# Kernel optimization log

Measured on AMD Instinct MI355X. Metric: run time of the kernel, lower is better.

## Reference

```python
import jax, jax.numpy as jnp
import numpy as np

B, J, D = 64, 512, 1024

def setup_inputs() -> dict:
    key = jax.random.key(0)
    k_x, k_m, k1, k2, k3 = jax.random.split(key, 5)
    x = jax.random.normal(k_x, (B, J, D), dtype=jnp.float32)
    mask = (jax.random.uniform(k_m, (B, J)) > 0.1).astype(jnp.float32)
    s1 = 1.0 / np.sqrt(D)
    W1 = jax.random.uniform(k1, (D, D), minval=-s1, maxval=s1, dtype=jnp.float32)
    b1 = jnp.zeros((D,), jnp.float32)
    W2 = jax.random.uniform(k2, (D, 1), minval=-s1, maxval=s1, dtype=jnp.float32)
    b2 = jnp.zeros((1,), jnp.float32)
    W3 = jax.random.uniform(k3, (D, 3), minval=-s1, maxval=s1, dtype=jnp.float32)
    b3 = jnp.zeros((3,), jnp.float32)
    return {"x": x, "mask": mask, "W1": W1, "b1": b1, "W2": W2, "b2": b2, "W3": W3, "b3": b3}

def reference(x, mask, W1, b1, W2, b2, W3, b3):
    # MLP attention scoring: linear1 -> tanh -> linear2 -> sigmoid
    h = jnp.tanh(jnp.einsum('bjd,de->bje', x, W1) + b1)          # [B,J,D]
    val = jax.nn.sigmoid(jnp.einsum('bjd,do->bjo', h, W2) + b2)  # [B,J,1]
    val = val * mask[:, :, None]                                  # mask out pads
    inv_sum = 1.0 / jnp.sum(val, axis=(1, 2))                     # [B]
    att_weights = val * inv_sum[:, None, None]                    # [B,J,1]
    pooled = jnp.einsum('bjk,bjm->bk', x, att_weights)            # [B,D]
    output_val = pooled @ W3 + b3                                 # [B,3]
    return output_val, att_weights
```

## Files before the change

kernel.cpp:

```cpp
#include <hip/hip_runtime.h>
#include <math.h>
#include <stdint.h>

#define B_ 64
#define J_ 512
#define D_ 1024

typedef __attribute__((ext_vector_type(8))) short short8;
typedef __attribute__((ext_vector_type(4))) float f32x4;

#define GLOBAL_AS __attribute__((address_space(1)))
#define LDS_AS    __attribute__((address_space(3)))

__device__ __forceinline__ void async16(const void* g, void* l) {
    __builtin_amdgcn_global_load_lds((const GLOBAL_AS uint32_t*)g,
                                     (LDS_AS uint32_t*)l, 16, 0, 0);
}

__device__ __forceinline__ float fast_tanh(float x) {
    return 1.0f - 2.0f / (1.0f + __expf(2.0f * x));
}

__device__ __forceinline__ uint32_t f2bf(float f) {
    uint32_t u = __builtin_bit_cast(uint32_t, f);
    u += 0x7fffu + ((u >> 16) & 1u);
    return u >> 16;
}
__device__ __forceinline__ uint32_t pack2(float lo, float hi) {
    return f2bf(lo) | (f2bf(hi) << 16);
}

__global__ __launch_bounds__(256) void transpose_cast_w1(const float* __restrict__ W1,
                                                         unsigned short* __restrict__ W1t) {
    __shared__ float t[32][33];
    const int n = blockIdx.x * 32 + threadIdx.x;
    for (int i = threadIdx.y; i < 32; i += 8)
        t[i][threadIdx.x] = W1[(size_t)(blockIdx.y * 32 + i) * D_ + n];
    __syncthreads();
    const int k = blockIdx.y * 32 + threadIdx.x;
    for (int i = threadIdx.y; i < 32; i += 8)
        W1t[(size_t)(blockIdx.x * 32 + i) * D_ + k] =
            (unsigned short)f2bf(t[threadIdx.x][i]);
}

__global__ __launch_bounds__(256, 2) void gemm_score_kernel(
    const float* __restrict__ x, const unsigned short* __restrict__ W1t,
    const float* __restrict__ b1, const float* __restrict__ W2,
    const float* __restrict__ b2, const float* __restrict__ mask,
    float* __restrict__ val_ws, float* __restrict__ pooled_part)
{
    __shared__ __align__(16) unsigned short ldsA[64 * 64];
    __shared__ __align__(16) unsigned short ldsB[256 * 64];
    __shared__ float pv_part[4][64];
    __shared__ float vrow[64];

    const int tid  = threadIdx.x;
    const int wave = tid >> 6;
    const int l    = tid & 63;
    const int l15  = l & 15;
    const int kgrp = l >> 4;
    const int l7   = l & 7;
    const int r0   = blockIdx.x * 64;

    const int ar = tid >> 3;
    const int ac = tid & 7;
    const float* gA0 = x + (size_t)(r0 + ar) * D_ + (ac << 3);
    const float* gA1 = gA0 + (size_t)32 * D_;
    uint4* dA0 = (uint4*)(ldsA + ar * 64 + ((ac ^ (ar & 7)) << 3));
    uint4* dA1 = (uint4*)(ldsA + (ar + 32) * 64 + ((ac ^ (ar & 7)) << 3));

    const int brl  = l >> 3;
    const int blog = (l & 7) ^ brl;
    size_t gBoff[8];
    unsigned short* lB[8];
    #pragma unroll
    for (int t = 0; t < 8; ++t) {
        const int row = t * 32 + wave * 8 + brl;
        gBoff[t] = (size_t)row * D_ + (blog << 3);
        lB[t] = ldsB + t * 2048 + wave * 512;
    }

    int aoff[4][2], boff[4][2];
    #pragma unroll
    for (int mi = 0; mi < 4; ++mi)
        #pragma unroll
        for (int ks = 0; ks < 2; ++ks)
            aoff[mi][ks] = (mi * 16 + l15) * 64 + (((ks * 4 + kgrp) ^ l7) << 3);
    #pragma unroll
    for (int ni = 0; ni < 4; ++ni)
        #pragma unroll
        for (int ks = 0; ks < 2; ++ks) {
            const int row = wave * 64 + ni * 16 + l15;
            boff[ni][ks] = row * 64 + (((ks * 4 + kgrp) ^ l7) << 3);
        }

    float pv[4][4];
    #pragma unroll
    for (int mi = 0; mi < 4; ++mi)
        #pragma unroll
        for (int r = 0; r < 4; ++r) pv[mi][r] = 0.f;

    for (int n0 = 0; n0 < 4; ++n0) {
        f32x4 acc[4][4];
        #pragma unroll
        for (int mi = 0; mi < 4; ++mi)
            #pragma unroll
            for (int ni = 0; ni < 4; ++ni)
                acc[mi][ni] = (f32x4){0.f, 0.f, 0.f, 0.f};

        const size_t nofs = (size_t)n0 * 256 * D_;
        for (int k0 = 0; k0 < D_; k0 += 64) {
            const float4 a00 = *reinterpret_cast<const float4*>(gA0 + k0);
            const float4 a01 = *reinterpret_cast<const float4*>(gA0 + k0 + 4);
            const float4 a10 = *reinterpret_cast<const float4*>(gA1 + k0);
            const float4 a11 = *reinterpret_cast<const float4*>(gA1 + k0 + 4);
            uint4 p0, p1;
            p0.x = pack2(a00.x, a00.y); p0.y = pack2(a00.z, a00.w);
            p0.z = pack2(a01.x, a01.y); p0.w = pack2(a01.z, a01.w);
            p1.x = pack2(a10.x, a10.y); p1.y = pack2(a10.z, a10.w);
            p1.z = pack2(a11.x, a11.y); p1.w = pack2(a11.z, a11.w);
            *dA0 = p0;
            *dA1 = p1;
            #pragma unroll
            for (int t = 0; t < 8; ++t)
                async16(W1t + nofs + gBoff[t] + k0, lB[t]);
            __syncthreads();

            #pragma unroll
            for (int ks = 0; ks < 2; ++ks) {
                short8 af[4], bfr[4];
                #pragma unroll
                for (int mi = 0; mi < 4; ++mi)
                    af[mi] = *reinterpret_cast<const short8*>(ldsA + aoff[mi][ks]);
                #pragma unroll
                for (int ni = 0; ni < 4; ++ni)
                    bfr[ni] = *reinterpret_cast<const short8*>(ldsB + boff[ni][ks]);
                #pragma unroll
                for (int mi = 0; mi < 4; ++mi)
                    #pragma unroll
                    for (int ni = 0; ni < 4; ++ni)
                        acc[mi][ni] = __builtin_amdgcn_mfma_f32_16x16x32_bf16(
                            af[mi], bfr[ni], acc[mi][ni], 0, 0, 0);
            }
            __syncthreads();
        }

        #pragma unroll
        for (int ni = 0; ni < 4; ++ni) {
            const int col = n0 * 256 + wave * 64 + ni * 16 + l15;
            const float b1v = b1[col];
            const float w2v = W2[col];
            #pragma unroll
            for (int mi = 0; mi < 4; ++mi)
                #pragma unroll
                for (int r = 0; r < 4; ++r) {
                    const float h = fast_tanh(acc[mi][ni][r] + b1v);
                    pv[mi][r] = fmaf(h, w2v, pv[mi][r]);
                }
        }
    }

    #pragma unroll
    for (int mi = 0; mi < 4; ++mi)
        #pragma unroll
        for (int r = 0; r < 4; ++r) {
            float s = pv[mi][r];
            s += __shfl_xor(s, 1);
            s += __shfl_xor(s, 2);
            s += __shfl_xor(s, 4);
            s += __shfl_xor(s, 8);
            if (l15 == 0) pv_part[wave][mi * 16 + kgrp * 4 + r] = s;
        }
    __syncthreads();
    if (tid < 64) {
        float s = b2[0];
        #pragma unroll
        for (int w = 0; w < 4; ++w) s += pv_part[w][tid];
        const float sg = 1.0f / (1.0f + __expf(-s));
        const float v = sg * mask[r0 + tid];
        val_ws[r0 + tid] = v;
        vrow[tid] = v;
    }
    __syncthreads();

    {
        const int kc = tid << 2;
        float a0 = 0.f, a1 = 0.f, a2 = 0.f, a3 = 0.f;
        for (int row = 0; row < 64; ++row) {
            const float v = vrow[row];
            const float4 xv = *reinterpret_cast<const float4*>(
                x + (size_t)(r0 + row) * D_ + kc);
            a0 = fmaf(xv.x, v, a0);
            a1 = fmaf(xv.y, v, a1);
            a2 = fmaf(xv.z, v, a2);
            a3 = fmaf(xv.w, v, a3);
        }
        *reinterpret_cast<float4*>(pooled_part + (size_t)blockIdx.x * D_ + kc) =
            make_float4(a0, a1, a2, a3);
    }
}

__global__ __launch_bounds__(256) void finalize_kernel(
    const float* __restrict__ val_ws, const float* __restrict__ pooled_part,
    const float* __restrict__ W3, const float* __restrict__ b3,
    float* __restrict__ out)
{
    __shared__ float sred[256];
    const int b = blockIdx.x;
    const int tid = threadIdx.x;

    const float v0 = val_ws[b * J_ + tid];
    const float v1 = val_ws[b * J_ + 256 + tid];
    sred[tid] = v0 + v1;
    __syncthreads();
    for (int s = 128; s > 0; s >>= 1) {
        if (tid < s) sred[tid] += sred[tid + s];
        __syncthreads();
    }
    const float inv = 1.0f / sred[0];

    out[192 + b * J_ + tid]       = v0 * inv;
    out[192 + b * J_ + 256 + tid] = v1 * inv;

    const int k = tid << 2;
    float acc3[3] = {0.f, 0.f, 0.f};
    #pragma unroll
    for (int c = 0; c < 4; ++c) {
        float p = 0.f;
        #pragma unroll
        for (int i = 0; i < 8; ++i)
            p += pooled_part[(size_t)(b * 8 + i) * D_ + k + c];
        p *= inv;
        acc3[0] = fmaf(p, W3[(k + c) * 3 + 0], acc3[0]);
        acc3[1] = fmaf(p, W3[(k + c) * 3 + 1], acc3[1]);
        acc3[2] = fmaf(p, W3[(k + c) * 3 + 2], acc3[2]);
    }
    for (int o = 0; o < 3; ++o) {
        __syncthreads();
        sred[tid] = acc3[o];
        __syncthreads();
        for (int s = 128; s > 0; s >>= 1) {
            if (tid < s) sred[tid] += sred[tid + s];
            __syncthreads();
        }
        if (tid == 0) out[b * 3 + o] = sred[0] + b3[o];
    }
}

extern "C" void kernel_launch(void* const* d_in, const int* in_sizes, int n_in,
                              void* d_out, int out_size, void* d_ws, size_t ws_size,
                              hipStream_t stream) {
    const float* x    = (const float*)d_in[0];
    const float* mask = (const float*)d_in[1];
    const float* W1   = (const float*)d_in[2];
    const float* b1   = (const float*)d_in[3];
    const float* W2   = (const float*)d_in[4];
    const float* b2   = (const float*)d_in[5];
    const float* W3   = (const float*)d_in[6];
    const float* b3   = (const float*)d_in[7];
    float* out = (float*)d_out;

    unsigned short* W1t = (unsigned short*)d_ws;
    float* val_ws       = (float*)((char*)d_ws + 2097152);
    float* pooled_part  = (float*)((char*)d_ws + 2097152 + 131072);

    transpose_cast_w1<<<dim3(32, 32), dim3(32, 8), 0, stream>>>(W1, W1t);
    gemm_score_kernel<<<512, 256, 0, stream>>>(x, W1t, b1, W2, b2, mask,
                                               val_ws, pooled_part);
    finalize_kernel<<<B_, 256, 0, stream>>>(val_ws, pooled_part, W3, b3, out);
}
```

Baseline: 321.1 us.

## Fuse finalize into GEMM via last-block counter, prefetch A, vectorize transpose

The separate finalize kernel is removed. The last of the 8 GEMM blocks per batch, found with an atomic counter that the transpose kernel zeroes, now does the normalization and the W3 projection. The A-tile global loads are software-prefetched one k-step ahead, so their latency overlaps the MFMA work. The W1 transpose/cast kernel now uses 64x64 tiles with float4 loads and 16-byte bf16 stores, and the per-tile B address arrays are collapsed into a single base pointer to free registers. The changes save one kernel launch at the cost of threadfences and an atomic, and the prefetch adds register pressure.

New measurement: 401.3 us. 1.25x slower.

```diff
diff --git a/kernel.cpp b/kernel.cpp
--- a/kernel.cpp
+++ b/kernel.cpp
@@ -30,29 +30,58 @@
     return f2bf(lo) | (f2bf(hi) << 16);
 }
 
-__global__ __launch_bounds__(256) void transpose_cast_w1(const float* __restrict__ W1,
-                                                         unsigned short* __restrict__ W1t) {
-    __shared__ float t[32][33];
-    const int n = blockIdx.x * 32 + threadIdx.x;
-    for (int i = threadIdx.y; i < 32; i += 8)
-        t[i][threadIdx.x] = W1[(size_t)(blockIdx.y * 32 + i) * D_ + n];
-    __syncthreads();
-    const int k = blockIdx.y * 32 + threadIdx.x;
-    for (int i = threadIdx.y; i < 32; i += 8)
-        W1t[(size_t)(blockIdx.x * 32 + i) * D_ + k] =
-            (unsigned short)f2bf(t[threadIdx.x][i]);
+__global__ __launch_bounds__(256) void transpose_cast_w1(
+    const float* __restrict__ W1, unsigned short* __restrict__ W1t,
+    unsigned int* __restrict__ cnt)
+{
+    if (blockIdx.x == 0 && blockIdx.y == 0 && threadIdx.x < B_)
+        cnt[threadIdx.x] = 0u;
+
+    __shared__ float t[64][65];
+    const int tx = threadIdx.x;
+    const int k0 = blockIdx.y * 64;
+    const int n0 = blockIdx.x * 64;
+
+    const int kr = tx >> 4;
+    const int c4 = (tx & 15) << 2;
+    #pragma unroll
+    for (int j = 0; j < 4; ++j) {
+        const float4 v = *reinterpret_cast<const float4*>(
+            &W1[(size_t)(k0 + kr + 16 * j) * D_ + n0 + c4]);
+        t[kr + 16 * j][c4 + 0] = v.x;
+        t[kr + 16 * j][c4 + 1] = v.y;
+        t[kr + 16 * j][c4 + 2] = v.z;
+        t[kr + 16 * j][c4 + 3] = v.w;
+    }
+    __syncthreads();
+
+    const int nl = tx >> 3;
+    const int k8 = (tx & 7) << 3;
+    #pragma unroll
+    for (int s = 0; s < 2; ++s) {
+        const int n = nl + 32 * s;
+        uint4 o;
+        o.x = pack2(t[k8 + 0][n], t[k8 + 1][n]);
+        o.y = pack2(t[k8 + 2][n], t[k8 + 3][n]);
+        o.z = pack2(t[k8 + 4][n], t[k8 + 5][n]);
+        o.w = pack2(t[k8 + 6][n], t[k8 + 7][n]);
+        *reinterpret_cast<uint4*>(&W1t[(size_t)(n0 + n) * D_ + k0 + k8]) = o;
+    }
 }
 
 __global__ __launch_bounds__(256, 2) void gemm_score_kernel(
     const float* __restrict__ x, const unsigned short* __restrict__ W1t,
     const float* __restrict__ b1, const float* __restrict__ W2,
     const float* __restrict__ b2, const float* __restrict__ mask,
-    float* __restrict__ val_ws, float* __restrict__ pooled_part)
+    const float* __restrict__ W3, const float* __restrict__ b3,
+    float* __restrict__ out, float* __restrict__ val_ws,
+    float* __restrict__ pooled_part, unsigned int* __restrict__ cnt)
 {
     __shared__ __align__(16) unsigned short ldsA[64 * 64];
     __shared__ __align__(16) unsigned short ldsB[256 * 64];
     __shared__ float pv_part[4][64];
     __shared__ float vrow[64];
+    __shared__ int lastflag;
 
     const int tid  = threadIdx.x;
     const int wave = tid >> 6;
@@ -61,6 +90,7 @@
     const int kgrp = l >> 4;
     const int l7   = l & 7;
     const int r0   = blockIdx.x * 64;
+    const int bb   = r0 >> 9;
 
     const int ar = tid >> 3;
     const int ac = tid & 7;
@@ -71,14 +101,8 @@
 
     const int brl  = l >> 3;
     const int blog = (l & 7) ^ brl;
-    size_t gBoff[8];
-    unsigned short* lB[8];
-    #pragma unroll
-    for (int t = 0; t < 8; ++t) {
-        const int row = t * 32 + wave * 8 + brl;
-        gBoff[t] = (size_t)row * D_ + (blog << 3);
-        lB[t] = ldsB + t * 2048 + wave * 512;
-    }
+    const unsigned short* gBbase = W1t + (size_t)(wave * 8 + brl) * D_ + (blog << 3);
+    unsigned short* lBbase = ldsB + wave * 512;
 
     int aoff[4][2], boff[4][2];
     #pragma unroll
@@ -100,6 +124,11 @@
         #pragma unroll
         for (int r = 0; r < 4; ++r) pv[mi][r] = 0.f;
 
+    float4 pa00 = *reinterpret_cast<const float4*>(gA0);
+    float4 pa01 = *reinterpret_cast<const float4*>(gA0 + 4);
+    float4 pa10 = *reinterpret_cast<const float4*>(gA1);
+    float4 pa11 = *reinterpret_cast<const float4*>(gA1 + 4);
+
     for (int n0 = 0; n0 < 4; ++n0) {
         f32x4 acc[4][4];
         #pragma unroll
@@ -110,21 +139,24 @@
 
         const size_t nofs = (size_t)n0 * 256 * D_;
         for (int k0 = 0; k0 < D_; k0 += 64) {
-            const float4 a00 = *reinterpret_cast<const float4*>(gA0 + k0);
-            const float4 a01 = *reinterpret_cast<const float4*>(gA0 + k0 + 4);
-            const float4 a10 = *reinterpret_cast<const float4*>(gA1 + k0);
-            const float4 a11 = *reinterpret_cast<const float4*>(gA1 + k0 + 4);
             uint4 p0, p1;
-            p0.x = pack2(a00.x, a00.y); p0.y = pack2(a00.z, a00.w);
-            p0.z = pack2(a01.x, a01.y); p0.w = pack2(a01.z, a01.w);
-            p1.x = pack2(a10.x, a10.y); p1.y = pack2(a10.z, a10.w);
-            p1.z = pack2(a11.x, a11.y); p1.w = pack2(a11.z, a11.w);
+            p0.x = pack2(pa00.x, pa00.y); p0.y = pack2(pa00.z, pa00.w);
+            p0.z = pack2(pa01.x, pa01.y); p0.w = pack2(pa01.z, pa01.w);
+            p1.x = pack2(pa10.x, pa10.y); p1.y = pack2(pa10.z, pa10.w);
+            p1.z = pack2(pa11.x, pa11.y); p1.w = pack2(pa11.z, pa11.w);
             *dA0 = p0;
             *dA1 = p1;
             #pragma unroll
             for (int t = 0; t < 8; ++t)
-                async16(W1t + nofs + gBoff[t] + k0, lB[t]);
-            __syncthreads();
+                async16(gBbase + nofs + (size_t)t * 32 * D_ + k0,
+                        lBbase + t * 2048);
+            __syncthreads();
+
+            const int nk = (k0 + 64) & (D_ - 1);
+            pa00 = *reinterpret_cast<const float4*>(gA0 + nk);
+            pa01 = *reinterpret_cast<const float4*>(gA0 + nk + 4);
+            pa10 = *reinterpret_cast<const float4*>(gA1 + nk);
+            pa11 = *reinterpret_cast<const float4*>(gA1 + nk + 4);
 
             #pragma unroll
             for (int ks = 0; ks < 2; ++ks) {
@@ -198,52 +230,57 @@
         *reinterpret_cast<float4*>(pooled_part + (size_t)blockIdx.x * D_ + kc) =
             make_float4(a0, a1, a2, a3);
     }
-}
-
-__global__ __launch_bounds__(256) void finalize_kernel(
-    const float* __restrict__ val_ws, const float* __restrict__ pooled_part,
-    const float* __restrict__ W3, const float* __restrict__ b3,
-    float* __restrict__ out)
-{
-    __shared__ float sred[256];
-    const int b = blockIdx.x;
-    const int tid = threadIdx.x;
-
-    const float v0 = val_ws[b * J_ + tid];
-    const float v1 = val_ws[b * J_ + 256 + tid];
-    sred[tid] = v0 + v1;
-    __syncthreads();
-    for (int s = 128; s > 0; s >>= 1) {
-        if (tid < s) sred[tid] += sred[tid + s];
-        __syncthreads();
-    }
-    const float inv = 1.0f / sred[0];
-
-    out[192 + b * J_ + tid]       = v0 * inv;
-    out[192 + b * J_ + 256 + tid] = v1 * inv;
-
-    const int k = tid << 2;
-    float acc3[3] = {0.f, 0.f, 0.f};
-    #pragma unroll
-    for (int c = 0; c < 4; ++c) {
-        float p = 0.f;
-        #pragma unroll
-        for (int i = 0; i < 8; ++i)
-            p += pooled_part[(size_t)(b * 8 + i) * D_ + k + c];
-        p *= inv;
-        acc3[0] = fmaf(p, W3[(k + c) * 3 + 0], acc3[0]);
-        acc3[1] = fmaf(p, W3[(k + c) * 3 + 1], acc3[1]);
-        acc3[2] = fmaf(p, W3[(k + c) * 3 + 2], acc3[2]);
-    }
-    for (int o = 0; o < 3; ++o) {
-        __syncthreads();
-        sred[tid] = acc3[o];
+
+    __threadfence();
+    __syncthreads();
+    if (tid == 0) {
+        const unsigned int old = atomicAdd(&cnt[bb], 1u);
+        lastflag = (old == 7u) ? 1 : 0;
+    }
+    __syncthreads();
+    if (!lastflag) return;
+    __threadfence();
+
+    {
+        float* sred = &pv_part[0][0];
+        const int b = bb;
+
+        const float v0 = val_ws[b * J_ + tid];
+        const float v1 = val_ws[b * J_ + 256 + tid];
+        sred[tid] = v0 + v1;
         __syncthreads();
         for (int s = 128; s > 0; s >>= 1) {
             if (tid < s) sred[tid] += sred[tid + s];
             __syncthreads();
         }
-        if (tid == 0) out[b * 3 + o] = sred[0] + b3[o];
+        const float inv = 1.0f / sred[0];
+
+        out[192 + b * J_ + tid]       = v0 * inv;
+        out[192 + b * J_ + 256 + tid] = v1 * inv;
+
+        const int k = tid << 2;
+        float acc3[3] = {0.f, 0.f, 0.f};
+        #pragma unroll
+        for (int c = 0; c < 4; ++c) {
+            float p = 0.f;
+            #pragma unroll
+            for (int i = 0; i < 8; ++i)
+                p += pooled_part[(size_t)(b * 8 + i) * D_ + k + c];
+            p *= inv;
+            acc3[0] = fmaf(p, W3[(k + c) * 3 + 0], acc3[0]);
+            acc3[1] = fmaf(p, W3[(k + c) * 3 + 1], acc3[1]);
+            acc3[2] = fmaf(p, W3[(k + c) * 3 + 2], acc3[2]);
+        }
+        for (int o = 0; o < 3; ++o) {
+            __syncthreads();
+            sred[tid] = acc3[o];
+            __syncthreads();
+            for (int s = 128; s > 0; s >>= 1) {
+                if (tid < s) sred[tid] += sred[tid + s];
+                __syncthreads();
+            }
+            if (tid == 0) out[b * 3 + o] = sred[0] + b3[o];
+        }
     }
 }
 
@@ -263,9 +300,9 @@
     unsigned short* W1t = (unsigned short*)d_ws;
     float* val_ws       = (float*)((char*)d_ws + 2097152);
     float* pooled_part  = (float*)((char*)d_ws + 2097152 + 131072);
-
-    transpose_cast_w1<<<dim3(32, 32), dim3(32, 8), 0, stream>>>(W1, W1t);
+    unsigned int* cnt   = (unsigned int*)((char*)d_ws + 2097152 + 131072 + 2097152);
+
+    transpose_cast_w1<<<dim3(16, 16), 256, 0, stream>>>(W1, W1t, cnt);
     gemm_score_kernel<<<512, 256, 0, stream>>>(x, W1t, b1, W2, b2, mask,
-                                               val_ws, pooled_part);
-    finalize_kernel<<<B_, 256, 0, stream>>>(val_ws, pooled_part, W3, b3, out);
-}
+                                               W3, b3, out, val_ws, pooled_part, cnt);
+}
```
